# Kernel tuning notes

Hardware: AMD Instinct MI355X
Metric: run time of the kernel (lower is better)

The kernel has to match this reference:

```python
import jax, jax.numpy as jnp
import numpy as np

B = 32
N = 1024  # half_size == num_delays == num_wavelength
DELTA_TAU = 1.5e-15
W_CENTER = 1.175e15  # center_frequency / 2
PULSE_THRESHOLD = 0.01
PENALTY = 10.0
REAL_W = 1.0; IMAG_W = 1.0; INT_W = 1.0; PHASE_W = 1.0; FROG_W = 1.0
MSE_WSUM = REAL_W + IMAG_W + INT_W + PHASE_W

# Hilbert mask exactly as in the torch source (even N branch): H[N//2+1:]=2, H[N//2]=1
_Hm = np.zeros(N, dtype=np.float32)
_Hm[N // 2 + 1:] = 2.0
_Hm[N // 2] = 1.0
HILBERT_MASK = jnp.asarray(_Hm)

# precomputed circular-shift gather indices: shifted[m, j] = x[(j - delay[m]) mod N]
_delays = np.arange(-(N // 2), N // 2)
SHIFT_IDX = jnp.asarray((np.arange(N)[None, :] - _delays[:, None]) % N)  # [N, N] int
SHIFT_FACTOR = jnp.exp(-1j * jnp.asarray(2.0 * W_CENTER * DELTA_TAU * _delays, dtype=jnp.float32)).astype(jnp.complex64)  # [N]


def hilbert(x):  # x: [N] real -> [N] complex analytical signal
    xf = jnp.fft.fft(x)
    return jnp.fft.ifft(xf * HILBERT_MASK)


def shg_mat(a):  # a: [N] complex -> [N, N] complex SHG matrix (vectorized createSHGmat)
    shifted = a[SHIFT_IDX]                                  # [N, N] all circular shifts
    rows = a[None, :] * shifted * SHIFT_FACTOR[None, :]     # elementwise complex multiply
    f = jnp.fft.fft(jnp.fft.fftshift(rows, axes=-1), axis=-1)  # one batched FFT
    return DELTA_TAU * jnp.fft.fftshift(f, axes=-1)


def _first_last(mask):  # mask: [B, N] bool -> per-sample first/last significant index with fallback
    any_m = jnp.any(mask, axis=1)
    first = jnp.where(any_m, jnp.argmax(mask, axis=1), 0)
    last = jnp.where(any_m, N - 1 - jnp.argmax(mask[:, ::-1], axis=1), N - 1)
    return first, last


def setup_inputs() -> dict:
    key = jax.random.key(0)
    k1, k2, k3 = jax.random.split(key, 3)
    prediction = jax.random.normal(k1, (B, N), dtype=jnp.float32)
    label = jax.random.normal(k2, (B, 2 * N), dtype=jnp.float32)
    shg_matrix = jax.random.uniform(k3, (B, 1, N, N), dtype=jnp.float32)
    return {"prediction": prediction, "label": label, "shg_matrix": shg_matrix}


def reference(prediction, label, shg_matrix):
    pa = jax.vmap(hilbert)(prediction)          # [B, N] complex64
    pr, pi = pa.real, pa.imag
    lr, li = label[:, :N], label[:, N:]
    l_int = lr ** 2 + li ** 2
    p_int = pr ** 2 + pi ** 2
    l_ph = jnp.arctan2(li, lr)
    p_ph = jnp.arctan2(pi, pr)

    # ---- FROG error ----
    shg_pred = jnp.abs(jax.vmap(shg_mat)(pa)) ** 2              # [B, N, N]
    shg_pred = shg_pred / jnp.max(shg_pred, axis=(1, 2), keepdims=True)  # normalizeSHGmatrix
    t_ref = shg_matrix[:, 0]                                    # [B, N, N]
    sum1 = jnp.sum(shg_pred * t_ref, axis=(1, 2))
    sum2 = jnp.sum(t_ref * t_ref, axis=(1, 2))
    mu = sum1 / sum2
    r = jnp.sum(shg_pred - mu[:, None, None] * t_ref, axis=(1, 2)) ** 2
    norm = (N * N) * jnp.max(shg_pred, axis=(1, 2)) ** 2
    frog = jnp.where(r == 0.0, 0.0, jnp.sqrt(r / norm))         # [B]

    # ---- weighted masked MSE ----
    fr, lr_idx = _first_last(jnp.abs(lr) > PULSE_THRESHOLD)
    fi, li_idx = _first_last(jnp.abs(li) > PULSE_THRESHOLD)
    first = jnp.minimum(fr, fi)
    last = jnp.maximum(lr_idx, li_idx)
    ar = jnp.arange(N)[None, :]
    in_range = (ar >= first[:, None]) & (ar < last[:, None])    # [first:last] slice semantics
    phase_mask = in_range.astype(jnp.float32)
    pulse_mask = jnp.where(in_range, PENALTY, 1.0)

    mse_real = jnp.mean((pr - lr) ** 2 * pulse_mask, axis=1) * REAL_W
    mse_imag = jnp.mean((pi - li) ** 2 * pulse_mask, axis=1) * IMAG_W
    mse_int = jnp.mean((p_int - l_int) ** 2 * pulse_mask, axis=1) * INT_W
    mse_ph = jnp.mean((p_ph - l_ph) ** 2 * phase_mask, axis=1) * PHASE_W
    mse = (mse_real + mse_imag + mse_int + mse_ph) / MSE_WSUM

    return jnp.mean(mse + FROG_W * frog)
```

## Files before the change

kernel.cpp:

```cpp
#include <hip/hip_runtime.h>
#include <math.h>

#define N 1024
#define BATCH 32
#define NT 256
#define ROWS 4
#define PADC(i) ((i) + ((i) >> 5))

#define WSYNC() asm volatile("s_waitcnt lgkmcnt(0)" ::: "memory")

typedef float2 cf;
__device__ __forceinline__ cf cadd(cf a, cf b){ return make_float2(a.x+b.x, a.y+b.y); }
__device__ __forceinline__ cf csub(cf a, cf b){ return make_float2(a.x-b.x, a.y-b.y); }
__device__ __forceinline__ cf cmul(cf a, cf b){ return make_float2(a.x*b.x - a.y*b.y, a.x*b.y + a.y*b.x); }

__device__ __forceinline__ cf twiddle(float jn){
    float s = __builtin_amdgcn_sinf(jn);
    float c = __builtin_amdgcn_cosf(jn);
    return make_float2(c, -s);
}

__device__ __forceinline__ int rev10(int m){
    int r = (int)(__brev((unsigned)m) >> 22);
    return ((r & 0x155) << 1) | ((r >> 1) & 0x155);
}

__device__ __forceinline__ void bfly(cf x0, cf x1, cf x2, cf x3,
                                     cf& y0, cf& y1, cf& y2, cf& y3){
    cf A = cadd(x0,x2), Bs = cadd(x1,x3);
    cf C = csub(x0,x2), D = csub(x1,x3);
    cf Dmi = make_float2(D.y, -D.x);
    y0 = cadd(A,Bs); y1 = cadd(C,Dmi); y2 = csub(A,Bs); y3 = csub(C,Dmi);
}

__device__ __forceinline__ void dif4h(cf* w, int base, int q, float jn){
    cf x0 = w[PADC(base)], x1 = w[PADC(base+q)], x2 = w[PADC(base+2*q)], x3 = w[PADC(base+3*q)];
    cf y0, y1, y2, y3; bfly(x0,x1,x2,x3,y0,y1,y2,y3);
    cf w1 = twiddle(jn), w2 = cmul(w1,w1), w3 = cmul(w2,w1);
    w[PADC(base)]     = y0;
    w[PADC(base+q)]   = cmul(y1,w1);
    w[PADC(base+2*q)] = cmul(y2,w2);
    w[PADC(base+3*q)] = cmul(y3,w3);
}
template<int LOG2N>
__device__ __forceinline__ void dif_stage(cf* w, int t){
    const int n = 1 << LOG2N, q = n >> 2;
    int j = t & (q - 1);
    int base = ((t >> (LOG2N - 2)) << LOG2N) + j;
    dif4h(w, base, q, (float)j * (1.0f / (float)n));
}
template<int LOG2N>
__device__ __forceinline__ void dit_stage(cf* w, int t){
    const int n = 1 << LOG2N, q = n >> 2;
    int j = t & (q - 1);
    int base = ((t >> (LOG2N - 2)) << LOG2N) + j;
    cf x0 = w[PADC(base)], x1 = w[PADC(base+q)], x2 = w[PADC(base+2*q)], x3 = w[PADC(base+3*q)];
    cf w1 = twiddle((float)j * (1.0f / (float)n));
    cf w2 = cmul(w1,w1), w3 = cmul(w2,w1);
    x1 = cmul(x1,w1); x2 = cmul(x2,w2); x3 = cmul(x3,w3);
    cf y0, y1, y2, y3; bfly(x0,x1,x2,x3,y0,y1,y2,y3);
    w[PADC(base)] = y0; w[PADC(base+q)] = y1; w[PADC(base+2*q)] = y2; w[PADC(base+3*q)] = y3;
}

__global__ __launch_bounds__(256) void hilbert_k(const float* __restrict__ pred,
                                                 const float* __restrict__ label,
                                                 cf* __restrict__ a,
                                                 cf* __restrict__ ca,
                                                 float* __restrict__ mseJ) {
    __shared__ cf wk[1056];
    __shared__ float rbuf[4][4];
    __shared__ int ibuf[4][4];
    __shared__ int s_first, s_last;
    int t = threadIdx.x, b = blockIdx.x;
    for (int i = t; i < N; i += 256) wk[PADC(i)] = make_float2(pred[b * N + i], 0.f);
    __syncthreads();
    dif_stage<10>(wk, t); __syncthreads();
    dif_stage<8>(wk, t);  __syncthreads();
    dif_stage<6>(wk, t);  __syncthreads();
    dif_stage<4>(wk, t);  __syncthreads();
    dif_stage<2>(wk, t);  __syncthreads();
    for (int i = t; i < N; i += 256) {
        int k = rev10(i);
        float f = (k < 512) ? 0.f : ((k == 512) ? 1.f : 2.f);
        cf v = wk[PADC(i)];
        wk[PADC(i)] = make_float2(f * v.x, -f * v.y);
    }
    __syncthreads();
    dit_stage<2>(wk, t);  __syncthreads();
    dit_stage<4>(wk, t);  __syncthreads();
    dit_stage<6>(wk, t);  __syncthreads();
    dit_stage<8>(wk, t);  __syncthreads();
    dit_stage<10>(wk, t); __syncthreads();
    const float sc = 1.f / (float)N;
    for (int i = t; i < N; i += 256) {
        cf v = wk[PADC(i)];
        cf av = make_float2(v.x * sc, -v.y * sc);
        wk[PADC(i)] = av;
        a[b * N + i] = av;
        float p = (float)(3.525 * (double)(i - 512));
        float s_, c_;
        sincosf(p, &s_, &c_);
        ca[b * N + i] = make_float2(av.x * c_ + av.y * s_, av.y * c_ - av.x * s_);
    }
    __syncthreads();

    int w = t >> 6, lane = t & 63;
    int mnR = N, mxR = -1, mnI = N, mxI = -1;
    for (int n = t; n < N; n += 256) {
        float lr = label[b * 2 * N + n];
        float li = label[b * 2 * N + N + n];
        if (fabsf(lr) > 0.01f) { mnR = min(mnR, n); mxR = max(mxR, n); }
        if (fabsf(li) > 0.01f) { mnI = min(mnI, n); mxI = max(mxI, n); }
    }
    for (int o = 32; o > 0; o >>= 1) {
        mnR = min(mnR, __shfl_down(mnR, o));
        mxR = max(mxR, __shfl_down(mxR, o));
        mnI = min(mnI, __shfl_down(mnI, o));
        mxI = max(mxI, __shfl_down(mxI, o));
    }
    if (lane == 0) { ibuf[w][0] = mnR; ibuf[w][1] = mxR; ibuf[w][2] = mnI; ibuf[w][3] = mxI; }
    __syncthreads();
    if (t == 0) {
        int a0 = N, a1 = -1, a2 = N, a3 = -1;
        for (int i = 0; i < 4; ++i) {
            a0 = min(a0, ibuf[i][0]); a1 = max(a1, ibuf[i][1]);
            a2 = min(a2, ibuf[i][2]); a3 = max(a3, ibuf[i][3]);
        }
        int fr   = (a0 == N) ? 0 : a0;
        int lstR = (a1 < 0) ? (N - 1) : a1;
        int fi   = (a2 == N) ? 0 : a2;
        int lstI = (a3 < 0) ? (N - 1) : a3;
        s_first = min(fr, fi);
        s_last  = max(lstR, lstI);
    }
    __syncthreads();
    int first = s_first, last = s_last;

    float m_r = 0.f, m_i = 0.f, m_n = 0.f, m_p = 0.f;
    for (int n = t; n < N; n += 256) {
        cf p = wk[PADC(n)];
        float lr = label[b * 2 * N + n];
        float li = label[b * 2 * N + N + n];
        bool in = (n >= first) && (n < last);
        float pm  = in ? 10.f : 1.f;
        float phm = in ? 1.f : 0.f;
        float dr = p.x - lr, di = p.y - li;
        float dn = (p.x * p.x + p.y * p.y) - (lr * lr + li * li);
        float dp = atan2f(p.y, p.x) - atan2f(li, lr);
        m_r += dr * dr * pm;
        m_i += di * di * pm;
        m_n += dn * dn * pm;
        m_p += dp * dp * phm;
    }
    for (int o = 32; o > 0; o >>= 1) {
        m_r += __shfl_down(m_r, o);
        m_i += __shfl_down(m_i, o);
        m_n += __shfl_down(m_n, o);
        m_p += __shfl_down(m_p, o);
    }
    if (lane == 0) { rbuf[w][0] = m_r; rbuf[w][1] = m_i; rbuf[w][2] = m_n; rbuf[w][3] = m_p; }
    __syncthreads();
    if (t == 0) {
        float s = 0.f;
        for (int i = 0; i < 4; ++i) s += rbuf[i][0] + rbuf[i][1] + rbuf[i][2] + rbuf[i][3];
        mseJ[b] = s * (1.f / (float)N) * 0.25f;
    }
}

__global__ __launch_bounds__(NT) void shg_k(const cf* __restrict__ a,
                                            const cf* __restrict__ cag,
                                            const float* __restrict__ tref,
                                            float* __restrict__ Praw,
                                            float* __restrict__ Prt,
                                            float* __restrict__ Pmax,
                                            float* __restrict__ Pt,
                                            float* __restrict__ Ptt) {
    __shared__ cf wk[ROWS * N];
    int t = threadIdx.x, blk = blockIdx.x;
    int b = blk >> 8;
    int dg = (blk & 255) << 2;
    const cf* arow  = a   + b * N;
    const cf* carow = cag + b * N;

    {
        int bt = t;
        cf w1 = twiddle((float)bt * (1.0f / 1024.0f));
        cf w2 = cmul(w1,w1), w3 = cmul(w2,w1);
        cf cv[4];
#pragma unroll
        for (int j = 0; j < 4; ++j) cv[j] = carow[bt + 256*j];
        int wb = bt ^ (((bt >> 4) & 7) << 1);
#pragma unroll
        for (int r = 0; r < ROWS; ++r) {
            int d = dg + r;
            cf x[4];
#pragma unroll
            for (int k = 0; k < 4; ++k)
                x[k] = cmul(cv[(k + 2) & 3], arow[(bt + 256*k - d) & 1023]);
            cf y0, y1, y2, y3; bfly(x[0],x[1],x[2],x[3],y0,y1,y2,y3);
            cf* w = wk + r * N + wb;
            w[0]   = y0;
            w[256] = cmul(y1,w1);
            w[512] = cmul(y2,w2);
            w[768] = cmul(y3,w3);
        }
    }
    __syncthreads();

    {
        int r  = t >> 6;
        int q2 = t & 63;
        int B2 = q2 >> 4;
        int v  = q2 & 15;
        cf* w = wk + r * N + B2 * 256;
        cf p[16];
#pragma unroll
        for (int m = 0; m < 16; ++m) p[m] = w[16*m + (v ^ ((m & 7) << 1))];
        {
            const cf T16 = { 0.923879533f, -0.382683432f };
            cf w1 = twiddle((float)v * (1.0f / 256.0f));
#pragma unroll
            for (int m0 = 0; m0 < 4; ++m0) {
                cf w2 = cmul(w1,w1), w3 = cmul(w2,w1);
                cf y0, y1, y2, y3;
                bfly(p[m0], p[m0+4], p[m0+8], p[m0+12], y0,y1,y2,y3);
                p[m0]    = y0;
                p[m0+4]  = cmul(y1,w1);
                p[m0+8]  = cmul(y2,w2);
                p[m0+12] = cmul(y3,w3);
                w1 = cmul(w1, T16);
            }
        }
        {
            cf w1 = twiddle((float)v * (1.0f / 64.0f));
            cf w2 = cmul(w1,w1), w3 = cmul(w2,w1);
#pragma unroll
            for (int s = 0; s < 4; ++s) {
                cf y0, y1, y2, y3;
                bfly(p[4*s], p[4*s+1], p[4*s+2], p[4*s+3], y0,y1,y2,y3);
                p[4*s]   = y0;
                p[4*s+1] = cmul(y1,w1);
                p[4*s+2] = cmul(y2,w2);
                p[4*s+3] = cmul(y3,w3);
            }
        }
#pragma unroll
        for (int m = 0; m < 16; ++m) w[16*m + (v ^ ((m & 7) << 1))] = p[m];
    }

    int r3 = t >> 6;
    int g  = t & 63;
    int bd = b * N + dg + r3;
    int kb = ((g & 3) << 4) | (g & 12) | (g >> 4);
    const float* trow2 = tref + ((size_t)bd << 10) + kb;
    float tv[16];
#pragma unroll
    for (int u = 0; u < 4; ++u)
#pragma unroll
        for (int m = 0; m < 4; ++m)
            tv[4*u + m] = trow2[(((m + 2) & 3) << 8) | (u << 6)];

    WSYNC();

    {
        const cf W1 = { 0.923879533f, -0.382683432f};
        const cf W2 = { 0.707106781f, -0.707106781f};
        const cf W3 = { 0.382683432f, -0.923879533f};
        const cf W6 = {-0.707106781f, -0.707106781f};
        const cf W9 = {-0.923879533f,  0.382683432f};
        cf* w = wk + r3 * N + 16 * g;
        int X = (g & 7) << 1;
        cf v[16];
#pragma unroll
        for (int j = 0; j < 8; ++j) {
            float4 q = *(const float4*)&w[(2*j) ^ X];
            v[2*j]   = make_float2(q.x, q.y);
            v[2*j+1] = make_float2(q.z, q.w);
        }
        cf o[16];
        bfly(v[0], v[4], v[8], v[12], o[0], o[4], o[8],  o[12]);
        { cf y0,y1,y2,y3; bfly(v[1],v[5],v[9], v[13],y0,y1,y2,y3);
          o[1]=y0; o[5]=cmul(y1,W1); o[9]=cmul(y2,W2); o[13]=cmul(y3,W3); }
        { cf y0,y1,y2,y3; bfly(v[2],v[6],v[10],v[14],y0,y1,y2,y3);
          o[2]=y0; o[6]=cmul(y1,W2); o[10]=make_float2(y2.y,-y2.x); o[14]=cmul(y3,W6); }
        { cf y0,y1,y2,y3; bfly(v[3],v[7],v[11],v[15],y0,y1,y2,y3);
          o[3]=y0; o[7]=cmul(y1,W3); o[11]=cmul(y2,W6); o[15]=cmul(y3,W9); }

        float sraw = 0.f, srt = 0.f, mx = 0.f, st = 0.f, stt = 0.f;
#pragma unroll
        for (int u = 0; u < 4; ++u) {
            cf y0, y1, y2, y3;
            bfly(o[4*u], o[4*u+1], o[4*u+2], o[4*u+3], y0, y1, y2, y3);
            cf ys[4] = {y0, y1, y2, y3};
#pragma unroll
            for (int m = 0; m < 4; ++m) {
                float m2 = ys[m].x * ys[m].x + ys[m].y * ys[m].y;
                float tvv = tv[4*u + m];
                sraw += m2;
                srt += m2 * tvv;
                mx = fmaxf(mx, m2);
                st += tvv;
                stt += tvv * tvv;
            }
        }
        for (int o_ = 32; o_ > 0; o_ >>= 1) {
            sraw += __shfl_down(sraw, o_);
            srt  += __shfl_down(srt, o_);
            mx    = fmaxf(mx, __shfl_down(mx, o_));
            st   += __shfl_down(st, o_);
            stt  += __shfl_down(stt, o_);
        }
        if ((t & 63) == 0) {
            Praw[bd] = sraw; Prt[bd] = srt; Pmax[bd] = mx; Pt[bd] = st; Ptt[bd] = stt;
        }
    }
}

__global__ __launch_bounds__(256) void loss_k(const float* __restrict__ Praw,
                                              const float* __restrict__ Prt,
                                              const float* __restrict__ Pmax,
                                              const float* __restrict__ Pt,
                                              const float* __restrict__ Ptt,
                                              const float* __restrict__ mseJ,
                                              float* __restrict__ out) {
    __shared__ float rbuf[4][8];
    int tid = threadIdx.x, b = blockIdx.x;
    int w = tid >> 6, lane = tid & 63;
    float sr = 0.f, srt = 0.f, mx = 0.f, st = 0.f, stt = 0.f;
    for (int i = tid; i < N; i += 256) {
        int idx = b * N + i;
        sr += Praw[idx]; srt += Prt[idx]; mx = fmaxf(mx, Pmax[idx]);
        st += Pt[idx];   stt += Ptt[idx];
    }
    for (int o = 32; o > 0; o >>= 1) {
        sr  += __shfl_down(sr, o);
        srt += __shfl_down(srt, o);
        mx   = fmaxf(mx, __shfl_down(mx, o));
        st  += __shfl_down(st, o);
        stt += __shfl_down(stt, o);
    }
    if (lane == 0) {
        rbuf[w][0] = sr; rbuf[w][1] = srt; rbuf[w][2] = mx;
        rbuf[w][3] = st; rbuf[w][4] = stt;
    }
    __syncthreads();
    if (tid == 0) {
        float A0 = 0.f, A1 = 0.f, A2 = 0.f, A3 = 0.f, A4 = 0.f;
        for (int i = 0; i < 4; ++i) {
            A0 += rbuf[i][0]; A1 += rbuf[i][1]; A2 = fmaxf(A2, rbuf[i][2]);
            A3 += rbuf[i][3]; A4 += rbuf[i][4];
        }
        float mu = (A1 / A2) / A4;
        float diff = A0 / A2 - mu * A3;
        float frog = fabsf(diff) * (1.f / (float)N);
        atomicAdd(out, (mseJ[b] + frog) * (1.f / (float)BATCH));
    }
}

extern "C" void kernel_launch(void* const* d_in, const int* in_sizes, int n_in,
                              void* d_out, int out_size, void* d_ws, size_t ws_size,
                              hipStream_t stream) {
    (void)in_sizes; (void)n_in; (void)out_size; (void)ws_size;
    const float* pred  = (const float*)d_in[0];
    const float* label = (const float*)d_in[1];
    const float* shg   = (const float*)d_in[2];
    float* out = (float*)d_out;

    char* ws = (char*)d_ws;
    cf* a   = (cf*)ws;
    cf* ca  = a + (size_t)BATCH * N;
    float* mseJ = (float*)(ca + (size_t)BATCH * N);
    float* P = mseJ + BATCH;
    float* Praw = P;
    float* Prt  = P + (size_t)BATCH * N;
    float* Pmax = P + 2 * (size_t)BATCH * N;
    float* Pt   = P + 3 * (size_t)BATCH * N;
    float* Ptt  = P + 4 * (size_t)BATCH * N;

    hipMemsetAsync(d_out, 0, sizeof(float), stream);
    hilbert_k<<<BATCH, 256, 0, stream>>>(pred, label, a, ca, mseJ);
    shg_k<<<BATCH * 256, NT, 0, stream>>>(a, ca, shg, Praw, Prt, Pmax, Pt, Ptt);
    loss_k<<<BATCH, 256, 0, stream>>>(Praw, Prt, Pmax, Pt, Ptt, mseJ, out);
}
```

Baseline: 229.0 us.

## Replace FFT Hilbert transform with direct cotangent convolution over more blocks

Computes the analytic signal with a direct discrete Hilbert convolution using a cotangent kernel on even/odd samples, instead of a forward FFT, mask and inverse FFT in shared memory. The real part becomes the mean-removed input. Work is spread over 8 single-wave blocks per sample instead of one 256-thread block, removing many block-wide barriers. Partial MSE sums per block are combined in the loss kernel. It trades O(N log N) work for O(N^2) MACs per sample and relies on the closed-form kernel matching the masked FFT.

```diff
diff --git a/kernel.cpp b/kernel.cpp
--- a/kernel.cpp
+++ b/kernel.cpp
@@ -5,7 +5,6 @@
 #define BATCH 32
 #define NT 256
 #define ROWS 4
-#define PADC(i) ((i) + ((i) >> 5))
 
 #define WSYNC() asm volatile("s_waitcnt lgkmcnt(0)" ::: "memory")
 
@@ -18,11 +17,6 @@
     float s = __builtin_amdgcn_sinf(jn);
     float c = __builtin_amdgcn_cosf(jn);
     return make_float2(c, -s);
-}
-
-__device__ __forceinline__ int rev10(int m){
-    int r = (int)(__brev((unsigned)m) >> 22);
-    return ((r & 0x155) << 1) | ((r >> 1) & 0x155);
 }
 
 __device__ __forceinline__ void bfly(cf x0, cf x1, cf x2, cf x3,
@@ -33,82 +27,73 @@
     y0 = cadd(A,Bs); y1 = cadd(C,Dmi); y2 = csub(A,Bs); y3 = csub(C,Dmi);
 }
 
-__device__ __forceinline__ void dif4h(cf* w, int base, int q, float jn){
-    cf x0 = w[PADC(base)], x1 = w[PADC(base+q)], x2 = w[PADC(base+2*q)], x3 = w[PADC(base+3*q)];
-    cf y0, y1, y2, y3; bfly(x0,x1,x2,x3,y0,y1,y2,y3);
-    cf w1 = twiddle(jn), w2 = cmul(w1,w1), w3 = cmul(w2,w1);
-    w[PADC(base)]     = y0;
-    w[PADC(base+q)]   = cmul(y1,w1);
-    w[PADC(base+2*q)] = cmul(y2,w2);
-    w[PADC(base+3*q)] = cmul(y3,w3);
-}
-template<int LOG2N>
-__device__ __forceinline__ void dif_stage(cf* w, int t){
-    const int n = 1 << LOG2N, q = n >> 2;
-    int j = t & (q - 1);
-    int base = ((t >> (LOG2N - 2)) << LOG2N) + j;
-    dif4h(w, base, q, (float)j * (1.0f / (float)n));
-}
-template<int LOG2N>
-__device__ __forceinline__ void dit_stage(cf* w, int t){
-    const int n = 1 << LOG2N, q = n >> 2;
-    int j = t & (q - 1);
-    int base = ((t >> (LOG2N - 2)) << LOG2N) + j;
-    cf x0 = w[PADC(base)], x1 = w[PADC(base+q)], x2 = w[PADC(base+2*q)], x3 = w[PADC(base+3*q)];
-    cf w1 = twiddle((float)j * (1.0f / (float)n));
-    cf w2 = cmul(w1,w1), w3 = cmul(w2,w1);
-    x1 = cmul(x1,w1); x2 = cmul(x2,w2); x3 = cmul(x3,w3);
-    cf y0, y1, y2, y3; bfly(x0,x1,x2,x3,y0,y1,y2,y3);
-    w[PADC(base)] = y0; w[PADC(base+q)] = y1; w[PADC(base+2*q)] = y2; w[PADC(base+3*q)] = y3;
-}
-
-__global__ __launch_bounds__(256) void hilbert_k(const float* __restrict__ pred,
-                                                 const float* __restrict__ label,
-                                                 cf* __restrict__ a,
-                                                 cf* __restrict__ ca,
-                                                 float* __restrict__ mseJ) {
-    __shared__ cf wk[1056];
-    __shared__ float rbuf[4][4];
-    __shared__ int ibuf[4][4];
-    __shared__ int s_first, s_last;
-    int t = threadIdx.x, b = blockIdx.x;
-    for (int i = t; i < N; i += 256) wk[PADC(i)] = make_float2(pred[b * N + i], 0.f);
-    __syncthreads();
-    dif_stage<10>(wk, t); __syncthreads();
-    dif_stage<8>(wk, t);  __syncthreads();
-    dif_stage<6>(wk, t);  __syncthreads();
-    dif_stage<4>(wk, t);  __syncthreads();
-    dif_stage<2>(wk, t);  __syncthreads();
-    for (int i = t; i < N; i += 256) {
-        int k = rev10(i);
-        float f = (k < 512) ? 0.f : ((k == 512) ? 1.f : 2.f);
-        cf v = wk[PADC(i)];
-        wk[PADC(i)] = make_float2(f * v.x, -f * v.y);
-    }
-    __syncthreads();
-    dit_stage<2>(wk, t);  __syncthreads();
-    dit_stage<4>(wk, t);  __syncthreads();
-    dit_stage<6>(wk, t);  __syncthreads();
-    dit_stage<8>(wk, t);  __syncthreads();
-    dit_stage<10>(wk, t); __syncthreads();
-    const float sc = 1.f / (float)N;
-    for (int i = t; i < N; i += 256) {
-        cf v = wk[PADC(i)];
-        cf av = make_float2(v.x * sc, -v.y * sc);
-        wk[PADC(i)] = av;
-        a[b * N + i] = av;
-        float p = (float)(3.525 * (double)(i - 512));
-        float s_, c_;
-        sincosf(p, &s_, &c_);
-        ca[b * N + i] = make_float2(av.x * c_ + av.y * s_, av.y * c_ - av.x * s_);
-    }
-    __syncthreads();
-
-    int w = t >> 6, lane = t & 63;
+__global__ __launch_bounds__(64) void hconv_k(const float* __restrict__ pred,
+                                              const float* __restrict__ label,
+                                              cf* __restrict__ a,
+                                              cf* __restrict__ ca,
+                                              float* __restrict__ mseP) {
+    __shared__ float xe[512], xo[512], C2[1024];
+    int l = threadIdx.x, blk = blockIdx.x;
+    int b = blk >> 3, oct = blk & 7;
+    const float* xr = pred + b * N;
+
+    float4 q0 = *(const float4*)(xr + 16 * l);
+    float4 q1 = *(const float4*)(xr + 16 * l + 4);
+    float4 q2 = *(const float4*)(xr + 16 * l + 8);
+    float4 q3 = *(const float4*)(xr + 16 * l + 12);
+    *(float4*)&xe[8 * l]     = make_float4(q0.x, q0.z, q1.x, q1.z);
+    *(float4*)&xe[8 * l + 4] = make_float4(q2.x, q2.z, q3.x, q3.z);
+    *(float4*)&xo[8 * l]     = make_float4(q0.y, q0.w, q1.y, q1.w);
+    *(float4*)&xo[8 * l + 4] = make_float4(q2.y, q2.w, q3.y, q3.w);
+    float lsum = q0.x+q0.y+q0.z+q0.w + q1.x+q1.y+q1.z+q1.w
+               + q2.x+q2.y+q2.z+q2.w + q3.x+q3.y+q3.z+q3.w;
+    for (int o = 32; o > 0; o >>= 1) lsum += __shfl_down(lsum, o);
+    float mean = __shfl(lsum, 0) * (1.f / 1024.f);
+
+#pragma unroll
+    for (int k = 0; k < 16; ++k) {
+        int u = l + 64 * k;
+        int j = u & 511;
+        float th = (float)(2 * j + 1) * (3.14159274f / 1024.f);
+        C2[u] = -(cosf(th) / sinf(th)) * (1.f / 512.f);
+    }
+    WSYNC();
+
+    int v = oct * 64 + l;
+    int P = v + 512;
+    float acc_e = 0.f, acc_o = 0.f;
+    float c_hi = C2[P];
+    for (int c = 0; c < 128; ++c) {
+        float4 xep = *(const float4*)&xe[4 * c];
+        float4 xop = *(const float4*)&xo[4 * c];
+        float c0 = C2[P - 1 - 4 * c];
+        float c1 = C2[P - 2 - 4 * c];
+        float c2 = C2[P - 3 - 4 * c];
+        float c3 = C2[P - 4 - 4 * c];
+        acc_e += xop.x * c0;  acc_o += xep.x * c_hi;
+        acc_e += xop.y * c1;  acc_o += xep.y * c0;
+        acc_e += xop.z * c2;  acc_o += xep.z * c1;
+        acc_e += xop.w * c3;  acc_o += xep.w * c2;
+        c_hi = c3;
+    }
+
+    int ne = 2 * v, no = ne + 1;
+    float axe = xe[v] - mean, axo = xo[v] - mean;
+    *(float4*)&a[b * N + ne] = make_float4(axe, acc_e, axo, acc_o);
+    float pe = (float)(3.525 * (double)(ne - 512));
+    float po = (float)(3.525 * (double)(no - 512));
+    float se, cE, so_, cO;
+    sincosf(pe, &se, &cE);
+    sincosf(po, &so_, &cO);
+    *(float4*)&ca[b * N + ne] = make_float4(axe * cE + acc_e * se, acc_e * cE - axe * se,
+                                            axo * cO + acc_o * so_, acc_o * cO - axo * so_);
+
+    const float* lab = label + b * 2 * N;
     int mnR = N, mxR = -1, mnI = N, mxI = -1;
-    for (int n = t; n < N; n += 256) {
-        float lr = label[b * 2 * N + n];
-        float li = label[b * 2 * N + N + n];
+#pragma unroll
+    for (int k = 0; k < 16; ++k) {
+        int n = l + 64 * k;
+        float lr = lab[n], li = lab[N + n];
         if (fabsf(lr) > 0.01f) { mnR = min(mnR, n); mxR = max(mxR, n); }
         if (fabsf(li) > 0.01f) { mnI = min(mnI, n); mxI = max(mxI, n); }
     }
@@ -118,53 +103,34 @@
         mnI = min(mnI, __shfl_down(mnI, o));
         mxI = max(mxI, __shfl_down(mxI, o));
     }
-    if (lane == 0) { ibuf[w][0] = mnR; ibuf[w][1] = mxR; ibuf[w][2] = mnI; ibuf[w][3] = mxI; }
-    __syncthreads();
-    if (t == 0) {
-        int a0 = N, a1 = -1, a2 = N, a3 = -1;
-        for (int i = 0; i < 4; ++i) {
-            a0 = min(a0, ibuf[i][0]); a1 = max(a1, ibuf[i][1]);
-            a2 = min(a2, ibuf[i][2]); a3 = max(a3, ibuf[i][3]);
-        }
-        int fr   = (a0 == N) ? 0 : a0;
-        int lstR = (a1 < 0) ? (N - 1) : a1;
-        int fi   = (a2 == N) ? 0 : a2;
-        int lstI = (a3 < 0) ? (N - 1) : a3;
-        s_first = min(fr, fi);
-        s_last  = max(lstR, lstI);
-    }
-    __syncthreads();
-    int first = s_first, last = s_last;
-
-    float m_r = 0.f, m_i = 0.f, m_n = 0.f, m_p = 0.f;
-    for (int n = t; n < N; n += 256) {
-        cf p = wk[PADC(n)];
-        float lr = label[b * 2 * N + n];
-        float li = label[b * 2 * N + N + n];
-        bool in = (n >= first) && (n < last);
-        float pm  = in ? 10.f : 1.f;
-        float phm = in ? 1.f : 0.f;
-        float dr = p.x - lr, di = p.y - li;
-        float dn = (p.x * p.x + p.y * p.y) - (lr * lr + li * li);
-        float dp = atan2f(p.y, p.x) - atan2f(li, lr);
-        m_r += dr * dr * pm;
-        m_i += di * di * pm;
-        m_n += dn * dn * pm;
-        m_p += dp * dp * phm;
-    }
-    for (int o = 32; o > 0; o >>= 1) {
-        m_r += __shfl_down(m_r, o);
-        m_i += __shfl_down(m_i, o);
-        m_n += __shfl_down(m_n, o);
-        m_p += __shfl_down(m_p, o);
-    }
-    if (lane == 0) { rbuf[w][0] = m_r; rbuf[w][1] = m_i; rbuf[w][2] = m_n; rbuf[w][3] = m_p; }
-    __syncthreads();
-    if (t == 0) {
-        float s = 0.f;
-        for (int i = 0; i < 4; ++i) s += rbuf[i][0] + rbuf[i][1] + rbuf[i][2] + rbuf[i][3];
-        mseJ[b] = s * (1.f / (float)N) * 0.25f;
-    }
+    mnR = __shfl(mnR, 0); mxR = __shfl(mxR, 0);
+    mnI = __shfl(mnI, 0); mxI = __shfl(mxI, 0);
+    int fr   = (mnR == N) ? 0 : mnR;
+    int lstR = (mxR < 0) ? (N - 1) : mxR;
+    int fi   = (mnI == N) ? 0 : mnI;
+    int lstI = (mxI < 0) ? (N - 1) : mxI;
+    int first = min(fr, fi), last = max(lstR, lstI);
+
+    float s_lane = 0.f;
+    {
+        float lr = lab[ne], li = lab[N + ne];
+        bool in = (ne >= first) && (ne < last);
+        float pm = in ? 10.f : 1.f, phm = in ? 1.f : 0.f;
+        float dr = axe - lr, di = acc_e - li;
+        float dn = (axe * axe + acc_e * acc_e) - (lr * lr + li * li);
+        float dp = atan2f(acc_e, axe) - atan2f(li, lr);
+        s_lane += (dr * dr + di * di + dn * dn) * pm + dp * dp * phm;
+
+        lr = lab[no]; li = lab[N + no];
+        in = (no >= first) && (no < last);
+        pm = in ? 10.f : 1.f; phm = in ? 1.f : 0.f;
+        dr = axo - lr; di = acc_o - li;
+        dn = (axo * axo + acc_o * acc_o) - (lr * lr + li * li);
+        dp = atan2f(acc_o, axo) - atan2f(li, lr);
+        s_lane += (dr * dr + di * di + dn * dn) * pm + dp * dp * phm;
+    }
+    for (int o = 32; o > 0; o >>= 1) s_lane += __shfl_down(s_lane, o);
+    if (l == 0) mseP[blk] = s_lane;
 }
 
 __global__ __launch_bounds__(NT) void shg_k(const cf* __restrict__ a,
@@ -321,7 +287,7 @@
                                               const float* __restrict__ Pmax,
                                               const float* __restrict__ Pt,
                                               const float* __restrict__ Ptt,
-                                              const float* __restrict__ mseJ,
+                                              const float* __restrict__ mseP,
                                               float* __restrict__ out) {
     __shared__ float rbuf[4][8];
     int tid = threadIdx.x, b = blockIdx.x;
@@ -353,7 +319,10 @@
         float mu = (A1 / A2) / A4;
         float diff = A0 / A2 - mu * A3;
         float frog = fabsf(diff) * (1.f / (float)N);
-        atomicAdd(out, (mseJ[b] + frog) * (1.f / (float)BATCH));
+        float ms = 0.f;
+        for (int k = 0; k < 8; ++k) ms += mseP[b * 8 + k];
+        ms *= (1.f / (float)N) * 0.25f;
+        atomicAdd(out, (ms + frog) * (1.f / (float)BATCH));
     }
 }
 
@@ -369,8 +338,8 @@
     char* ws = (char*)d_ws;
     cf* a   = (cf*)ws;
     cf* ca  = a + (size_t)BATCH * N;
-    float* mseJ = (float*)(ca + (size_t)BATCH * N);
-    float* P = mseJ + BATCH;
+    float* mseP = (float*)(ca + (size_t)BATCH * N);
+    float* P = mseP + BATCH * 8;
     float* Praw = P;
     float* Prt  = P + (size_t)BATCH * N;
     float* Pmax = P + 2 * (size_t)BATCH * N;
@@ -378,7 +347,7 @@
     float* Ptt  = P + 4 * (size_t)BATCH * N;
 
     hipMemsetAsync(d_out, 0, sizeof(float), stream);
-    hilbert_k<<<BATCH, 256, 0, stream>>>(pred, label, a, ca, mseJ);
+    hconv_k<<<BATCH * 8, 64, 0, stream>>>(pred, label, a, ca, mseP);
     shg_k<<<BATCH * 256, NT, 0, stream>>>(a, ca, shg, Praw, Prt, Pmax, Pt, Ptt);
-    loss_k<<<BATCH, 256, 0, stream>>>(Praw, Prt, Pmax, Pt, Ptt, mseJ, out);
-}
+    loss_k<<<BATCH, 256, 0, stream>>>(Praw, Prt, Pmax, Pt, Ptt, mseP, out);
+}
```

Result: slower. 233.7 us (+2.1%).
